# Kernel tuning notes

Measured on AMD Instinct MI355X. Metric: run time of the kernel, lower is better.

The kernel has to match this reference:

```python
import jax, jax.numpy as jnp
import numpy as np

DEN_LEAKY = 1e-05
NUM_LEAKY = 1e-20


def _chain_objf(xexp, lengths, e_in, e_out, e_pdf, e_prob, leaky, final, coeff):
    """Leaky-HMM forward recursion (pychain forward_backward objective).

    xexp: [B,T,D] exp'd clamped network outputs
    e_*:  edge lists, either shared [E] or per-utterance [B,E]
    leaky/final: [S] or [B,S]
    Returns scalar objf = sum_b log p(X_b | graph_b).
    """
    B, T, D = xexp.shape
    if leaky.ndim == 1:
        leaky = jnp.broadcast_to(leaky[None, :], (B, leaky.shape[0]))
        final = jnp.broadcast_to(final[None, :], (B, final.shape[0]))
    S = leaky.shape[1]
    if e_in.ndim == 1:
        E = e_in.shape[0]
        e_in = jnp.broadcast_to(e_in[None, :], (B, E))
        e_out = jnp.broadcast_to(e_out[None, :], (B, E))
        e_pdf = jnp.broadcast_to(e_pdf[None, :], (B, E))
        e_prob = jnp.broadcast_to(e_prob[None, :], (B, E))
    seg = (e_out + S * jnp.arange(B, dtype=e_out.dtype)[:, None]).ravel()

    # alpha at t=0: mass 1 on start_state (0), plus leaky mass (alpha_sum = 1)
    alpha0 = jnp.zeros((B, S), xexp.dtype).at[:, 0].set(1.0)
    alpha0 = alpha0 + coeff * leaky

    mask_t = jnp.arange(T)[:, None] < lengths[None, :]  # [T,B] ragged frame mask

    def step(carry, inp):
        alpha, logz = carry
        xt, m = inp  # xt: [B,D], m: [B]
        # transition scores: alpha[src] * graph_prob * exp_logit[pdf]
        vals = (jnp.take_along_axis(alpha, e_in, axis=1)
                * e_prob
                * jnp.take_along_axis(xt, e_pdf, axis=1))  # [B,E]
        anew = jax.ops.segment_sum(vals.ravel(), seg, num_segments=B * S).reshape(B, S)
        asum = anew.sum(-1, keepdims=True)  # [B,1] per-frame arbitrary scale
        adash = (anew + coeff * leaky * asum) / asum  # leaky-HMM + renorm
        alpha = jnp.where(m[:, None], adash, alpha)
        logz = logz + jnp.where(m, jnp.log(asum[:, 0]), 0.0)
        return (alpha, logz), None

    (alpha, logz), _ = jax.lax.scan(
        step, (alpha0, jnp.zeros((B,), xexp.dtype)),
        (jnp.transpose(xexp, (1, 0, 2)), mask_t))
    return jnp.sum(logz + jnp.log(jnp.sum(alpha * final, axis=-1)))


def setup_inputs() -> dict:
    key = jax.random.key(0)
    ks = jax.random.split(key, 12)
    B, T, D = 32, 400, 2048
    S_den, E_den = 2000, 60000
    S_num, E_num = 512, 2048
    x = jax.random.normal(ks[0], (B, T, D), dtype=jnp.float32)
    x_lengths = jnp.clip(T - jnp.arange(B, dtype=jnp.int32) * 8, 32, T)  # sorted desc
    den_e_in = jax.random.randint(ks[1], (E_den,), 0, S_den, dtype=jnp.int32)
    den_e_out = jax.random.randint(ks[2], (E_den,), 0, S_den, dtype=jnp.int32)
    den_e_pdf = jax.random.randint(ks[3], (E_den,), 0, D, dtype=jnp.int32)
    den_e_prob = jax.random.uniform(ks[4], (E_den,), dtype=jnp.float32, minval=0.05, maxval=1.0)
    den_leaky = jax.random.uniform(ks[5], (S_den,), dtype=jnp.float32, minval=0.01, maxval=1.0)
    den_final = jax.random.uniform(ks[6], (S_den,), dtype=jnp.float32, minval=0.1, maxval=1.0)
    num_e_in = jax.random.randint(ks[7], (B, E_num), 0, S_num, dtype=jnp.int32)
    num_e_out = jax.random.randint(ks[8], (B, E_num), 0, S_num, dtype=jnp.int32)
    num_e_pdf = jax.random.randint(ks[9], (B, E_num), 0, D, dtype=jnp.int32)
    num_e_prob = jax.random.uniform(ks[10], (B, E_num), dtype=jnp.float32, minval=0.05, maxval=1.0)
    k11, k12 = jax.random.split(ks[11])
    num_leaky = jax.random.uniform(k11, (B, S_num), dtype=jnp.float32, minval=0.01, maxval=1.0)
    num_final = jax.random.uniform(k12, (B, S_num), dtype=jnp.float32, minval=0.1, maxval=1.0)
    return {"x": x, "x_lengths": x_lengths,
            "den_e_in": den_e_in, "den_e_out": den_e_out, "den_e_pdf": den_e_pdf,
            "den_e_prob": den_e_prob, "den_leaky": den_leaky, "den_final": den_final,
            "num_e_in": num_e_in, "num_e_out": num_e_out, "num_e_pdf": num_e_pdf,
            "num_e_prob": num_e_prob, "num_leaky": num_leaky, "num_final": num_final}


def reference(x, x_lengths, den_e_in, den_e_out, den_e_pdf, den_e_prob, den_leaky,
              den_final, num_e_in, num_e_out, num_e_pdf, num_e_prob, num_leaky,
              num_final):
    xexp = jnp.exp(jnp.clip(x, -30.0, 30.0))
    den_objf = _chain_objf(xexp, x_lengths, den_e_in, den_e_out, den_e_pdf,
                           den_e_prob, den_leaky, den_final, DEN_LEAKY)
    num_objf = _chain_objf(xexp, x_lengths, num_e_in, num_e_out, num_e_pdf,
                           num_e_prob, num_leaky, num_final, NUM_LEAKY)
    objf = -(num_objf - den_objf)
    return objf / x_lengths.sum().astype(x.dtype)
```

## Files before the change

### kernel.cpp

```cpp
#include <hip/hip_runtime.h>
#include <math.h>

#define B_SZ   32
#define T_SZ   400
#define D_SZ   2048
#define S_DEN  2000
#define E_DEN  60000
#define S_NUM  512
#define E_NUM  2048
#define DEN_C  1e-5f
#define NUM_C  1e-20f

#define P_CH   4
#define NTHR   512
#define EPT    32
#define EPC    16384

#define REC_OFF     0u
#define ANEWG_OFF   0u
#define PACK_OFF    960000u
#define ROWPTR_OFF  1484288u
#define CNT_OFF     1492352u
#define SROW_OFF    1492352u
#define CUR_OFF     1500352u
#define RSPLIT_OFF  1508352u
#define PSUM_OFF    1508416u
#define CTR_OFF     1509440u
#define TOTD_OFF    1509568u
#define TOTN_OFF    1509696u
#define WS_BYTES    1509824u

__device__ __forceinline__ float expclip(float v) {
    return __expf(fminf(fmaxf(v, -30.f), 30.f));
}
__device__ __forceinline__ float ldf_agent(const float* p) {
    return __hip_atomic_load(p, __ATOMIC_RELAXED, __HIP_MEMORY_SCOPE_AGENT);
}
__device__ __forceinline__ int ldi_agent(const int* p) {
    return __hip_atomic_load(p, __ATOMIC_RELAXED, __HIP_MEMORY_SCOPE_AGENT);
}
__device__ __forceinline__ void stf_agent(float* p, float v) {
    __hip_atomic_store(p, v, __ATOMIC_RELAXED, __HIP_MEMORY_SCOPE_AGENT);
}

__global__ void prep_init(char* ws) {
    int tid = threadIdx.x;
    int* cnt = (int*)(ws + CNT_OFF);
    int* cur = (int*)(ws + CUR_OFF);
    for (int i = tid; i < S_DEN; i += 256) { cnt[i] = 0; cur[i] = 0; }
    if (tid < B_SZ) ((int*)(ws + CTR_OFF))[tid] = 0;
}

__global__ void prep_hist(const int* __restrict__ e_out, char* ws) {
    int e = blockIdx.x * blockDim.x + threadIdx.x;
    if (e < E_DEN) atomicAdd((int*)(ws + CNT_OFF) + e_out[e], 1);
}

__global__ __launch_bounds__(1024) void prep_scan(char* ws) {
    __shared__ int sb[2][2048];
    const int* cnt = (const int*)(ws + CNT_OFF);
    int* rowp = (int*)(ws + ROWPTR_OFF);
    int tid = threadIdx.x;
    for (int i = tid; i < 2048; i += 1024) sb[0][i] = (i < S_DEN) ? cnt[i] : 0;
    __syncthreads();
    int cur = 0;
    for (int d = 1; d < 2048; d <<= 1) {
        for (int i = tid; i < 2048; i += 1024)
            sb[1 - cur][i] = sb[cur][i] + ((i >= d) ? sb[cur][i - d] : 0);
        __syncthreads();
        cur ^= 1;
    }
    if (tid == 0) rowp[0] = 0;
    for (int i = tid; i < S_DEN; i += 1024) rowp[i + 1] = sb[cur][i];
    __syncthreads();
    if (tid == 0) {
        int* rs = (int*)(ws + RSPLIT_OFF);
        rs[0] = 0; rs[P_CH] = S_DEN;
        for (int p = 1; p < P_CH; ++p) {
            int target = (E_DEN / P_CH) * p;
            int lo = 0, hi = S_DEN;
            while (lo < hi) {
                int mid = (lo + hi) >> 1;
                int v = (mid == 0) ? 0 : sb[cur][mid - 1];
                if (v >= target) hi = mid; else lo = mid + 1;
            }
            rs[p] = lo;
        }
    }
}

__global__ void prep_scatter(const int* __restrict__ e_in, const int* __restrict__ e_out,
                             const int* __restrict__ e_pdf, const float* __restrict__ e_prob,
                             char* ws) {
    int e = blockIdx.x * blockDim.x + threadIdx.x;
    if (e >= E_DEN) return;
    const int* rowp = (const int*)(ws + ROWPTR_OFF);
    int* cur = (int*)(ws + CUR_OFF);
    int4* recs = (int4*)(ws + REC_OFF);
    int o = e_out[e];
    int pos = rowp[o] + atomicAdd(&cur[o], 1);
    int4 r;
    r.x = e_in[e]; r.y = e_pdf[e];
    r.z = __float_as_int(e_prob[e]);
    r.w = o;
    recs[pos] = r;
}

__global__ void prep_pack(char* ws) {
    int slot = blockIdx.x * blockDim.x + threadIdx.x;
    if (slot >= P_CH * EPC) return;
    int p = slot >> 14;
    int k = slot & (EPC - 1);
    const int* rowp = (const int*)(ws + ROWPTR_OFF);
    const int* rs = (const int*)(ws + RSPLIT_OFF);
    int ebase = rowp[rs[p]], eend = rowp[rs[p + 1]];
    uint2* pk = (uint2*)(ws + PACK_OFF);
    int idx = ebase + k;
    uint2 val;
    int myrow;
    if (idx < eend) {
        const int4* r4 = (const int4*)(ws + REC_OFF);
        int4 r = r4[idx];
        myrow = r.w;
        int nxt = (idx + 1 < eend) ? r4[idx + 1].w : myrow;
        unsigned d = (unsigned)(nxt - myrow);
        if (d > 1023u) d = 1023u;
        val = make_uint2((unsigned)r.x | ((unsigned)r.y << 11) | (d << 22),
                         (unsigned)r.z);
    } else {
        val = make_uint2(0u, 0u);
        myrow = rs[p];
    }
    pk[slot] = val;
    if ((k & (EPT - 1)) == 0)
        ((int*)(ws + SROW_OFF))[(p << 9) + (k >> 5)] = myrow;
}

__global__ __launch_bounds__(NTHR, 2) void chain_fwd3(
    const float* __restrict__ x, const int* __restrict__ lengths,
    const float* __restrict__ den_leaky, const float* __restrict__ den_final,
    const int* __restrict__ num_in, const int* __restrict__ num_out,
    const int* __restrict__ num_pdf, const float* __restrict__ num_prob,
    const float* __restrict__ num_leaky, const float* __restrict__ num_final,
    char* __restrict__ ws)
{
    __shared__ float alpha[2048];
    __shared__ float xrow[2048];
    __shared__ float anew[2048];
    __shared__ float red[8];
    extern __shared__ float dynpad[];
    const int tid = threadIdx.x;
    if (lengths[0] == -12345) dynpad[tid] = 1.f;

    if (blockIdx.x < P_CH * B_SZ) {
        const int b = blockIdx.x & (B_SZ - 1);
        const int p = blockIdx.x >> 5;
        const int len = lengths[b];
        const float* xb = x + (size_t)b * T_SZ * D_SZ;
        const int* rs = (const int*)(ws + RSPLIT_OFF);
        const int rlo = rs[p], rhi = rs[p + 1];
        float* anewg = (float*)(ws + ANEWG_OFF) + ((size_t)(b << 1) << 11);
        float* psumg = (float*)(ws + PSUM_OFF);
        int* ctr = (int*)(ws + CTR_OFF) + b;

        float lc[4], fc[4];
        #pragma unroll
        for (int i = 0; i < 4; ++i) {
            int s = tid + (i << 9);
            lc[i] = (s < S_DEN) ? DEN_C * den_leaky[s] : 0.f;
            fc[i] = (s < S_DEN) ? den_final[s] : 0.f;
        }
        #pragma unroll
        for (int i = 0; i < 4; ++i) {
            int s = tid + (i << 9);
            alpha[s] = lc[i] + ((s == 0) ? 1.f : 0.f);
            anew[s] = 0.f;
            xrow[s] = expclip(xb[s]);
        }

        const uint4* __restrict__ pk4 = (const uint4*)(ws + PACK_OFF);
        const int qb = (p << 13) + (tid << 4);
        const int row0 = ((const int*)(ws + SROW_OFF))[(p << 9) + tid];
        float logz = 0.f;
        uint4 c0 = pk4[qb + 0], c1 = pk4[qb + 1], c2 = pk4[qb + 2], c3 = pk4[qb + 3];
        uint4 c4 = pk4[qb + 4], c5 = pk4[qb + 5], c6 = pk4[qb + 6], c7 = pk4[qb + 7];
        __syncthreads();

        for (int t = 0; t < len; ++t) {
            const int tn = (t + 1 < len) ? t + 1 : t;
            const float* xq = xb + (size_t)tn * D_SZ;
            const float xn0 = xq[tid], xn1 = xq[tid + 512];
            const float xn2 = xq[tid + 1024], xn3 = xq[tid + 1536];

            float acc = 0.f, psum = 0.f;
            int row = row0;
            #pragma unroll
            for (int sb = 0; sb < 2; ++sb) {
                const int nq = qb + (((sb + 1) & 1) << 3);
                uint4 n0 = pk4[nq + 0], n1 = pk4[nq + 1], n2 = pk4[nq + 2], n3 = pk4[nq + 3];
                uint4 n4 = pk4[nq + 4], n5 = pk4[nq + 5], n6 = pk4[nq + 6], n7 = pk4[nq + 7];
                const unsigned w[16] = {c0.x, c0.z, c1.x, c1.z, c2.x, c2.z, c3.x, c3.z,
                                        c4.x, c4.z, c5.x, c5.z, c6.x, c6.z, c7.x, c7.z};
                const unsigned pr[16] = {c0.y, c0.w, c1.y, c1.w, c2.y, c2.w, c3.y, c3.w,
                                         c4.y, c4.w, c5.y, c5.w, c6.y, c6.w, c7.y, c7.w};
                float av[16], xv[16];
                #pragma unroll
                for (int i = 0; i < 16; ++i) av[i] = alpha[w[i] & 2047u];
                #pragma unroll
                for (int i = 0; i < 16; ++i) xv[i] = xrow[(w[i] >> 11) & 2047u];
                #pragma unroll
                for (int i = 0; i < 16; ++i) {
                    acc = __fmaf_rn(av[i] * __uint_as_float(pr[i]), xv[i], acc);
                    const unsigned d = w[i] >> 22;
                    if (d) { psum += acc; atomicAdd(&anew[row], acc); acc = 0.f; row += (int)d; }
                }
                c0 = n0; c1 = n1; c2 = n2; c3 = n3;
                c4 = n4; c5 = n5; c6 = n6; c7 = n7;
            }
            psum += acc;
            if (acc != 0.f) atomicAdd(&anew[row], acc);

            #pragma unroll
            for (int o = 32; o > 0; o >>= 1) psum += __shfl_down(psum, o, 64);
            if ((tid & 63) == 0) red[tid >> 6] = psum;
            __syncthreads();

            float* ag = anewg + ((t & 1) << 11);
            const int pbase = ((b << 1) | (t & 1)) * P_CH;
            if (tid == 0) {
                float bs = 0.f;
                #pragma unroll
                for (int i = 0; i < 8; ++i) bs += red[i];
                stf_agent(&psumg[pbase + p], bs);
            }
            for (int r = rlo + tid; r < rhi; r += NTHR) { stf_agent(&ag[r], anew[r]); anew[r] = 0.f; }
            asm volatile("s_waitcnt vmcnt(0)" ::: "memory");
            __syncthreads();
            if (tid == 0) {
                __hip_atomic_fetch_add(ctr, 1, __ATOMIC_RELAXED, __HIP_MEMORY_SCOPE_AGENT);
                const int target = P_CH * (t + 1);
                int guard = 0;
                while (ldi_agent(ctr) < target) {
                    __builtin_amdgcn_s_sleep(2);
                    if (++guard > (1 << 17)) break;
                }
            }
            __syncthreads();

            float asum = 0.f;
            #pragma unroll
            for (int q = 0; q < P_CH; ++q) asum += ldf_agent(&psumg[pbase + q]);
            const float inv = 1.f / asum;

            #pragma unroll
            for (int i = 0; i < 4; ++i) {
                const int s = tid + (i << 9);
                float an = (s < S_DEN) ? ldf_agent(&ag[s]) : 0.f;
                alpha[s] = __fmaf_rn(an, inv, lc[i]);
            }
            xrow[tid]        = expclip(xn0);
            xrow[tid + 512]  = expclip(xn1);
            xrow[tid + 1024] = expclip(xn2);
            xrow[tid + 1536] = expclip(xn3);
            logz += logf(asum);
            __syncthreads();
        }

        if (p == 0) {
            float fs = alpha[tid] * fc[0] + alpha[tid + 512] * fc[1]
                     + alpha[tid + 1024] * fc[2] + alpha[tid + 1536] * fc[3];
            #pragma unroll
            for (int o = 32; o > 0; o >>= 1) fs += __shfl_down(fs, o, 64);
            if ((tid & 63) == 0) red[tid >> 6] = fs;
            __syncthreads();
            if (tid == 0) {
                float tot = 0.f;
                #pragma unroll
                for (int i = 0; i < 8; ++i) tot += red[i];
                ((float*)(ws + TOTD_OFF))[b] = logz + logf(tot);
            }
        }
    } else {
        const int b = blockIdx.x - P_CH * B_SZ;
        const int len = lengths[b];
        const float* xb = x + (size_t)b * T_SZ * D_SZ;
        float* nalpha = alpha;
        float* nanew  = anew;
        const float lk = num_leaky[(b << 9) + tid];
        const float fn = num_final[(b << 9) + tid];
        int ein[4], eout[4], epdf[4]; float eprb[4];
        #pragma unroll
        for (int k = 0; k < 4; ++k) {
            int e = (b << 11) + tid + (k << 9);
            ein[k] = num_in[e]; eout[k] = num_out[e];
            epdf[k] = num_pdf[e]; eprb[k] = num_prob[e];
        }
        nalpha[tid] = NUM_C * lk + ((tid == 0) ? 1.f : 0.f);
        nanew[tid] = 0.f;
        #pragma unroll
        for (int i = 0; i < 4; ++i) xrow[tid + (i << 9)] = expclip(xb[tid + (i << 9)]);
        float logz = 0.f;
        __syncthreads();

        for (int t = 0; t < len; ++t) {
            const int tn = (t + 1 < len) ? t + 1 : t;
            const float* xq = xb + (size_t)tn * D_SZ;
            const float xn0 = xq[tid], xn1 = xq[tid + 512];
            const float xn2 = xq[tid + 1024], xn3 = xq[tid + 1536];
            #pragma unroll
            for (int k = 0; k < 4; ++k) {
                float v = nalpha[ein[k]] * eprb[k] * xrow[epdf[k]];
                atomicAdd(&nanew[eout[k]], v);
            }
            __syncthreads();
            float ps = nanew[tid];
            #pragma unroll
            for (int o = 32; o > 0; o >>= 1) ps += __shfl_down(ps, o, 64);
            if ((tid & 63) == 0) red[tid >> 6] = ps;
            __syncthreads();
            float asum = 0.f;
            #pragma unroll
            for (int i = 0; i < 8; ++i) asum += red[i];
            nalpha[tid] = __fmaf_rn(NUM_C * lk, asum, nanew[tid]) * (1.f / asum);
            nanew[tid] = 0.f;
            xrow[tid]        = expclip(xn0);
            xrow[tid + 512]  = expclip(xn1);
            xrow[tid + 1024] = expclip(xn2);
            xrow[tid + 1536] = expclip(xn3);
            logz += logf(asum);
            __syncthreads();
        }
        float fs = nalpha[tid] * fn;
        #pragma unroll
        for (int o = 32; o > 0; o >>= 1) fs += __shfl_down(fs, o, 64);
        if ((tid & 63) == 0) red[tid >> 6] = fs;
        __syncthreads();
        if (tid == 0) {
            float tot = 0.f;
            #pragma unroll
            for (int i = 0; i < 8; ++i) tot += red[i];
            ((float*)(ws + TOTN_OFF))[b] = logz + logf(tot);
        }
    }
}

__global__ void combine2(const char* __restrict__ ws, const int* __restrict__ lengths,
                         float* __restrict__ out) {
    const float* totd = (const float*)(ws + TOTD_OFF);
    const float* totn = (const float*)(ws + TOTN_OFF);
    int tid = threadIdx.x;
    float v = 0.f, l = 0.f;
    if (tid < B_SZ) { v = totd[tid] - totn[tid]; l = (float)lengths[tid]; }
    #pragma unroll
    for (int o = 32; o > 0; o >>= 1) { v += __shfl_down(v, o, 64); l += __shfl_down(l, o, 64); }
    if (tid == 0) out[0] = v / l;
}

__global__ __launch_bounds__(1024) void chain_fwd_kernel(
    const float* __restrict__ x, const int* __restrict__ lengths,
    const int* __restrict__ den_in, const int* __restrict__ den_out,
    const int* __restrict__ den_pdf, const float* __restrict__ den_prob,
    const float* __restrict__ den_leaky, const float* __restrict__ den_final,
    const int* __restrict__ num_in, const int* __restrict__ num_out,
    const int* __restrict__ num_pdf, const float* __restrict__ num_prob,
    const float* __restrict__ num_leaky, const float* __restrict__ num_final,
    float* __restrict__ part)
{
    __shared__ float xrow[D_SZ];
    __shared__ float alpha[S_DEN];
    __shared__ float anew[S_DEN];
    __shared__ float red[17];
    const int tid = threadIdx.x;
    const int nthr = 1024;
    const bool is_den = blockIdx.x < B_SZ;
    const int b = blockIdx.x & (B_SZ - 1);
    int S, E;
    const int *e_in, *e_out, *e_pdf;
    const float *e_prob, *leaky, *fin;
    float coeff;
    if (is_den) {
        S = S_DEN; E = E_DEN;
        e_in = den_in; e_out = den_out; e_pdf = den_pdf; e_prob = den_prob;
        leaky = den_leaky; fin = den_final; coeff = DEN_C;
    } else {
        S = S_NUM; E = E_NUM;
        e_in = num_in + b * E_NUM; e_out = num_out + b * E_NUM;
        e_pdf = num_pdf + b * E_NUM; e_prob = num_prob + b * E_NUM;
        leaky = num_leaky + b * S_NUM; fin = num_final + b * S_NUM;
        coeff = NUM_C;
    }
    const int len = lengths[b];
    const float* xb = x + (size_t)b * T_SZ * D_SZ;
    for (int s = tid; s < S; s += nthr)
        alpha[s] = coeff * leaky[s] + (s == 0 ? 1.0f : 0.0f);
    float logz = 0.0f;
    for (int t = 0; t < len; ++t) {
        for (int s = tid; s < S; s += nthr) anew[s] = 0.0f;
        const float* xt = xb + (size_t)t * D_SZ;
        for (int d = tid; d < D_SZ; d += nthr)
            xrow[d] = __expf(fminf(fmaxf(xt[d], -30.0f), 30.0f));
        __syncthreads();
        for (int e = tid; e < E; e += nthr) {
            float v = alpha[e_in[e]] * e_prob[e] * xrow[e_pdf[e]];
            atomicAdd(&anew[e_out[e]], v);
        }
        __syncthreads();
        float ps = 0.0f;
        for (int s = tid; s < S; s += nthr) ps += anew[s];
        #pragma unroll
        for (int off = 32; off > 0; off >>= 1) ps += __shfl_down(ps, off, 64);
        if ((tid & 63) == 0) red[tid >> 6] = ps;
        __syncthreads();
        if (tid < 64) {
            float v = (tid < 16) ? red[tid] : 0.0f;
            #pragma unroll
            for (int off = 8; off > 0; off >>= 1) v += __shfl_down(v, off, 64);
            if (tid == 0) red[16] = v;
        }
        __syncthreads();
        const float asum = red[16];
        const float inv = 1.0f / asum;
        for (int s = tid; s < S; s += nthr)
            alpha[s] = (anew[s] + coeff * leaky[s] * asum) * inv;
        logz += logf(asum);
        __syncthreads();
    }
    float fs = 0.0f;
    for (int s = tid; s < S; s += nthr) fs += alpha[s] * fin[s];
    #pragma unroll
    for (int off = 32; off > 0; off >>= 1) fs += __shfl_down(fs, off, 64);
    if ((tid & 63) == 0) red[tid >> 6] = fs;
    __syncthreads();
    if (tid < 64) {
        float v = (tid < 16) ? red[tid] : 0.0f;
        #pragma unroll
        for (int off = 8; off > 0; off >>= 1) v += __shfl_down(v, off, 64);
        if (tid == 0) part[blockIdx.x] = logz + logf(v);
    }
}

__global__ void combine_kernel(const float* __restrict__ part,
                               const int* __restrict__ lengths,
                               float* __restrict__ out)
{
    int tid = threadIdx.x;
    float v = 0.0f, l = 0.0f;
    if (tid < B_SZ) { v = part[tid] - part[B_SZ + tid]; l = (float)lengths[tid]; }
    #pragma unroll
    for (int off = 32; off > 0; off >>= 1) { v += __shfl_down(v, off, 64); l += __shfl_down(l, off, 64); }
    if (tid == 0) out[0] = v / l;
}

extern "C" void kernel_launch(void* const* d_in, const int* in_sizes, int n_in,
                              void* d_out, int out_size, void* d_ws, size_t ws_size,
                              hipStream_t stream)
{
    const float* x          = (const float*)d_in[0];
    const int*   lengths    = (const int*)  d_in[1];
    const int*   den_in_p   = (const int*)  d_in[2];
    const int*   den_out_p  = (const int*)  d_in[3];
    const int*   den_pdf_p  = (const int*)  d_in[4];
    const float* den_prob_p = (const float*)d_in[5];
    const float* den_leaky  = (const float*)d_in[6];
    const float* den_final  = (const float*)d_in[7];
    const int*   num_in_p   = (const int*)  d_in[8];
    const int*   num_out_p  = (const int*)  d_in[9];
    const int*   num_pdf_p  = (const int*)  d_in[10];
    const float* num_prob_p = (const float*)d_in[11];
    const float* num_leaky  = (const float*)d_in[12];
    const float* num_final  = (const float*)d_in[13];

    if (ws_size >= WS_BYTES) {
        char* ws = (char*)d_ws;
        hipLaunchKernelGGL(prep_init, dim3(1), dim3(256), 0, stream, ws);
        hipLaunchKernelGGL(prep_hist, dim3((E_DEN + 255) / 256), dim3(256), 0, stream,
                           den_out_p, ws);
        hipLaunchKernelGGL(prep_scan, dim3(1), dim3(1024), 0, stream, ws);
        hipLaunchKernelGGL(prep_scatter, dim3((E_DEN + 255) / 256), dim3(256), 0, stream,
                           den_in_p, den_out_p, den_pdf_p, den_prob_p, ws);
        hipLaunchKernelGGL(prep_pack, dim3((P_CH * EPC + 255) / 256), dim3(256), 0, stream, ws);
        hipLaunchKernelGGL(chain_fwd3, dim3(P_CH * B_SZ + B_SZ), dim3(NTHR), 60000, stream,
                           x, lengths, den_leaky, den_final,
                           num_in_p, num_out_p, num_pdf_p, num_prob_p,
                           num_leaky, num_final, ws);
        hipLaunchKernelGGL(combine2, dim3(1), dim3(64), 0, stream,
                           ws, lengths, (float*)d_out);
    } else {
        float* part = (float*)d_ws;
        hipLaunchKernelGGL(chain_fwd_kernel, dim3(2 * B_SZ), dim3(1024), 0, stream,
                           x, lengths,
                           den_in_p, den_out_p, den_pdf_p, den_prob_p, den_leaky, den_final,
                           num_in_p, num_out_p, num_pdf_p, num_prob_p, num_leaky, num_final,
                           part);
        hipLaunchKernelGGL(combine_kernel, dim3(1), dim3(64), 0, stream,
                           part, lengths, (float*)d_out);
    }
}
```

Baseline: 2.785 ms.

## Interleave two utterances per denominator block with per-block ready flags

Each denominator block now runs the recursion for a pair of utterances in lockstep. It does both edge passes before waiting on the cross-block partial sums, so the wait for one utterance is hidden behind work on the other. The shared arrival counter is replaced by per-partition monotonic step flags, and the partial sums are polled by a few lanes. This halves the number of denominator blocks and doubles shared-memory state per block. The loop runs for the first utterance's length, so it assumes the second utterance in each pair is no longer than the first.

```diff
diff --git a/kernel.cpp b/kernel.cpp
--- a/kernel.cpp
+++ b/kernel.cpp
@@ -12,6 +12,7 @@
 #define NUM_C  1e-20f
 
 #define P_CH   4
+#define PGRP   16
 #define NTHR   512
 #define EPT    32
 #define EPC    16384
@@ -25,10 +26,10 @@
 #define CUR_OFF     1500352u
 #define RSPLIT_OFF  1508352u
 #define PSUM_OFF    1508416u
-#define CTR_OFF     1509440u
-#define TOTD_OFF    1509568u
-#define TOTN_OFF    1509696u
-#define WS_BYTES    1509824u
+#define FLAG_OFF    1509440u
+#define TOTD_OFF    1509952u
+#define TOTN_OFF    1510080u
+#define WS_BYTES    1510208u
 
 __device__ __forceinline__ float expclip(float v) {
     return __expf(fminf(fmaxf(v, -30.f), 30.f));
@@ -40,6 +41,9 @@
     return __hip_atomic_load(p, __ATOMIC_RELAXED, __HIP_MEMORY_SCOPE_AGENT);
 }
 __device__ __forceinline__ void stf_agent(float* p, float v) {
+    __hip_atomic_store(p, v, __ATOMIC_RELAXED, __HIP_MEMORY_SCOPE_AGENT);
+}
+__device__ __forceinline__ void sti_agent(int* p, int v) {
     __hip_atomic_store(p, v, __ATOMIC_RELAXED, __HIP_MEMORY_SCOPE_AGENT);
 }
 
@@ -48,7 +52,8 @@
     int* cnt = (int*)(ws + CNT_OFF);
     int* cur = (int*)(ws + CUR_OFF);
     for (int i = tid; i < S_DEN; i += 256) { cnt[i] = 0; cur[i] = 0; }
-    if (tid < B_SZ) ((int*)(ws + CTR_OFF))[tid] = 0;
+    int* flags = (int*)(ws + FLAG_OFF);
+    if (tid < B_SZ * P_CH) flags[tid] = 0;
 }
 
 __global__ void prep_hist(const int* __restrict__ e_out, char* ws) {
@@ -136,7 +141,41 @@
         ((int*)(ws + SROW_OFF))[(p << 9) + (k >> 5)] = myrow;
 }
 
-__global__ __launch_bounds__(NTHR, 2) void chain_fwd3(
+#define EDGE_PASS(ALD, XLD, NLD)                                               \
+  {                                                                            \
+    float acc = 0.f, psum = 0.f;                                               \
+    int row = row0;                                                            \
+    _Pragma("unroll")                                                          \
+    for (int sb = 0; sb < 2; ++sb) {                                           \
+      const int nq = qb + (((sb + 1) & 1) << 3);                               \
+      uint4 n0 = pk4[nq + 0], n1 = pk4[nq + 1], n2 = pk4[nq + 2], n3 = pk4[nq + 3]; \
+      uint4 n4 = pk4[nq + 4], n5 = pk4[nq + 5], n6 = pk4[nq + 6], n7 = pk4[nq + 7]; \
+      const unsigned w[16] = {c0.x, c0.z, c1.x, c1.z, c2.x, c2.z, c3.x, c3.z,  \
+                              c4.x, c4.z, c5.x, c5.z, c6.x, c6.z, c7.x, c7.z}; \
+      const unsigned pr[16] = {c0.y, c0.w, c1.y, c1.w, c2.y, c2.w, c3.y, c3.w, \
+                               c4.y, c4.w, c5.y, c5.w, c6.y, c6.w, c7.y, c7.w};\
+      float av[16], xv[16];                                                    \
+      _Pragma("unroll")                                                        \
+      for (int i = 0; i < 16; ++i) av[i] = (ALD)[w[i] & 2047u];                \
+      _Pragma("unroll")                                                        \
+      for (int i = 0; i < 16; ++i) xv[i] = (XLD)[(w[i] >> 11) & 2047u];        \
+      _Pragma("unroll")                                                        \
+      for (int i = 0; i < 16; ++i) {                                           \
+        acc = __fmaf_rn(av[i] * __uint_as_float(pr[i]), xv[i], acc);           \
+        const unsigned d = w[i] >> 22;                                         \
+        if (d) { psum += acc; atomicAdd(&(NLD)[row], acc); acc = 0.f; row += (int)d; } \
+      }                                                                        \
+      c0 = n0; c1 = n1; c2 = n2; c3 = n3;                                      \
+      c4 = n4; c5 = n5; c6 = n6; c7 = n7;                                      \
+    }                                                                          \
+    psum += acc;                                                               \
+    if (acc != 0.f) atomicAdd(&(NLD)[row], acc);                               \
+    _Pragma("unroll")                                                          \
+    for (int o = 32; o > 0; o >>= 1) psum += __shfl_down(psum, o, 64);         \
+    if ((tid & 63) == 0) red[tid >> 6] = psum;                                 \
+  }
+
+__global__ __launch_bounds__(NTHR, 2) void chain_fwd4(
     const float* __restrict__ x, const int* __restrict__ lengths,
     const float* __restrict__ den_leaky, const float* __restrict__ den_final,
     const int* __restrict__ num_in, const int* __restrict__ num_out,
@@ -144,24 +183,26 @@
     const float* __restrict__ num_leaky, const float* __restrict__ num_final,
     char* __restrict__ ws)
 {
-    __shared__ float alpha[2048];
-    __shared__ float xrow[2048];
-    __shared__ float anew[2048];
-    __shared__ float red[8];
+    __shared__ float sAlpha[2][2048];
+    __shared__ float sXrow[2][2048];
+    __shared__ float sAnew[2][2048];
+    __shared__ float red[16];
     extern __shared__ float dynpad[];
     const int tid = threadIdx.x;
     if (lengths[0] == -12345) dynpad[tid] = 1.f;
 
-    if (blockIdx.x < P_CH * B_SZ) {
-        const int b = blockIdx.x & (B_SZ - 1);
-        const int p = blockIdx.x >> 5;
-        const int len = lengths[b];
-        const float* xb = x + (size_t)b * T_SZ * D_SZ;
+    if (blockIdx.x < P_CH * PGRP) {
+        const int g = blockIdx.x & (PGRP - 1);
+        const int p = blockIdx.x >> 4;
+        const int bA = 2 * g, bB = 2 * g + 1;
+        const int lenA = lengths[bA], lenB = lengths[bB];
+        const float* xA = x + (size_t)bA * T_SZ * D_SZ;
+        const float* xB = x + (size_t)bB * T_SZ * D_SZ;
         const int* rs = (const int*)(ws + RSPLIT_OFF);
         const int rlo = rs[p], rhi = rs[p + 1];
-        float* anewg = (float*)(ws + ANEWG_OFF) + ((size_t)(b << 1) << 11);
+        float* anewg = (float*)(ws + ANEWG_OFF);
         float* psumg = (float*)(ws + PSUM_OFF);
-        int* ctr = (int*)(ws + CTR_OFF) + b;
+        int* flags   = (int*)(ws + FLAG_OFF);
 
         float lc[4], fc[4];
         #pragma unroll
@@ -173,119 +214,152 @@
         #pragma unroll
         for (int i = 0; i < 4; ++i) {
             int s = tid + (i << 9);
-            alpha[s] = lc[i] + ((s == 0) ? 1.f : 0.f);
-            anew[s] = 0.f;
-            xrow[s] = expclip(xb[s]);
+            float a0 = lc[i] + ((s == 0) ? 1.f : 0.f);
+            sAlpha[0][s] = a0; sAlpha[1][s] = a0;
+            sAnew[0][s] = 0.f; sAnew[1][s] = 0.f;
+            sXrow[0][s] = expclip(xA[s]);
+            sXrow[1][s] = expclip(xB[s]);
         }
 
         const uint4* __restrict__ pk4 = (const uint4*)(ws + PACK_OFF);
         const int qb = (p << 13) + (tid << 4);
         const int row0 = ((const int*)(ws + SROW_OFF))[(p << 9) + tid];
-        float logz = 0.f;
+        float logzA = 0.f, logzB = 0.f;
         uint4 c0 = pk4[qb + 0], c1 = pk4[qb + 1], c2 = pk4[qb + 2], c3 = pk4[qb + 3];
         uint4 c4 = pk4[qb + 4], c5 = pk4[qb + 5], c6 = pk4[qb + 6], c7 = pk4[qb + 7];
         __syncthreads();
 
-        for (int t = 0; t < len; ++t) {
-            const int tn = (t + 1 < len) ? t + 1 : t;
-            const float* xq = xb + (size_t)tn * D_SZ;
-            const float xn0 = xq[tid], xn1 = xq[tid + 512];
-            const float xn2 = xq[tid + 1024], xn3 = xq[tid + 1536];
-
-            float acc = 0.f, psum = 0.f;
-            int row = row0;
+        for (int t = 0; t < lenA; ++t) {
+            const bool haveB = (t < lenB);
+            const int par = t & 1;
+
+            const int tnA = (t + 1 < lenA) ? t + 1 : t;
+            const float* xqA = xA + (size_t)tnA * D_SZ;
+            const float xa0 = xqA[tid],        xa1 = xqA[tid + 512];
+            const float xa2 = xqA[tid + 1024], xa3 = xqA[tid + 1536];
+            float xb0 = 0.f, xb1 = 0.f, xb2 = 0.f, xb3 = 0.f;
+            if (haveB) {
+                const int tnB = (t + 1 < lenB) ? t + 1 : t;
+                const float* xqB = xB + (size_t)tnB * D_SZ;
+                xb0 = xqB[tid];        xb1 = xqB[tid + 512];
+                xb2 = xqB[tid + 1024]; xb3 = xqB[tid + 1536];
+            }
+
+            EDGE_PASS(sAlpha[0], sXrow[0], sAnew[0]);
+            __syncthreads();
+            {
+                float* ag = anewg + (size_t)(((bA << 1) | par) << 11);
+                if (tid == 0) {
+                    float bs = red[0]+red[1]+red[2]+red[3]+red[4]+red[5]+red[6]+red[7];
+                    stf_agent(&psumg[(((bA << 1) | par) << 2) + p], bs);
+                }
+                for (int r = rlo + tid; r < rhi; r += NTHR) {
+                    stf_agent(&ag[r], sAnew[0][r]); sAnew[0][r] = 0.f;
+                }
+                asm volatile("s_waitcnt vmcnt(0)" ::: "memory");
+            }
+            __syncthreads();
+            if (tid == 0) sti_agent(&flags[(bA << 2) + p], t + 1);
+
+            if (haveB) {
+                EDGE_PASS(sAlpha[1], sXrow[1], sAnew[1]);
+                __syncthreads();
+                {
+                    float* ag = anewg + (size_t)(((bB << 1) | par) << 11);
+                    if (tid == 0) {
+                        float bs = red[0]+red[1]+red[2]+red[3]+red[4]+red[5]+red[6]+red[7];
+                        stf_agent(&psumg[(((bB << 1) | par) << 2) + p], bs);
+                    }
+                    for (int r = rlo + tid; r < rhi; r += NTHR) {
+                        stf_agent(&ag[r], sAnew[1][r]); sAnew[1][r] = 0.f;
+                    }
+                    asm volatile("s_waitcnt vmcnt(0)" ::: "memory");
+                }
+                __syncthreads();
+                if (tid == 0) sti_agent(&flags[(bB << 2) + p], t + 1);
+            }
+
+            sXrow[0][tid]        = expclip(xa0);
+            sXrow[0][tid + 512]  = expclip(xa1);
+            sXrow[0][tid + 1024] = expclip(xa2);
+            sXrow[0][tid + 1536] = expclip(xa3);
+            if (haveB) {
+                sXrow[1][tid]        = expclip(xb0);
+                sXrow[1][tid + 512]  = expclip(xb1);
+                sXrow[1][tid + 1024] = expclip(xb2);
+                sXrow[1][tid + 1536] = expclip(xb3);
+            }
+
+            if (tid < 4) {
+                const int fi = (bA << 2) + tid; int gd = 0;
+                while (ldi_agent(&flags[fi]) < t + 1) {
+                    __builtin_amdgcn_s_sleep(1);
+                    if (++gd > (1 << 15)) break;
+                }
+                red[8 + tid] = ldf_agent(&psumg[(((bA << 1) | par) << 2) + tid]);
+            } else if (haveB && tid >= 64 && tid < 68) {
+                const int q = tid - 64;
+                const int fi = (bB << 2) + q; int gd = 0;
+                while (ldi_agent(&flags[fi]) < t + 1) {
+                    __builtin_amdgcn_s_sleep(1);
+                    if (++gd > (1 << 15)) break;
+                }
+                red[12 + q] = ldf_agent(&psumg[(((bB << 1) | par) << 2) + q]);
+            }
+            __syncthreads();
+
+            {
+                const float asum = red[8] + red[9] + red[10] + red[11];
+                const float inv = 1.f / asum;
+                const float* ag = anewg + (size_t)(((bA << 1) | par) << 11);
+                #pragma unroll
+                for (int i = 0; i < 4; ++i) {
+                    const int s = tid + (i << 9);
+                    float an = (s < S_DEN) ? ldf_agent(&ag[s]) : 0.f;
+                    sAlpha[0][s] = __fmaf_rn(an, inv, lc[i]);
+                }
+                logzA += logf(asum);
+            }
+            if (haveB) {
+                const float asum = red[12] + red[13] + red[14] + red[15];
+                const float inv = 1.f / asum;
+                const float* ag = anewg + (size_t)(((bB << 1) | par) << 11);
+                #pragma unroll
+                for (int i = 0; i < 4; ++i) {
+                    const int s = tid + (i << 9);
+                    float an = (s < S_DEN) ? ldf_agent(&ag[s]) : 0.f;
+                    sAlpha[1][s] = __fmaf_rn(an, inv, lc[i]);
+                }
+                logzB += logf(asum);
+            }
+            __syncthreads();
+        }
+
+        if (p == 0) {
             #pragma unroll
-            for (int sb = 0; sb < 2; ++sb) {
-                const int nq = qb + (((sb + 1) & 1) << 3);
-                uint4 n0 = pk4[nq + 0], n1 = pk4[nq + 1], n2 = pk4[nq + 2], n3 = pk4[nq + 3];
-                uint4 n4 = pk4[nq + 4], n5 = pk4[nq + 5], n6 = pk4[nq + 6], n7 = pk4[nq + 7];
-                const unsigned w[16] = {c0.x, c0.z, c1.x, c1.z, c2.x, c2.z, c3.x, c3.z,
-                                        c4.x, c4.z, c5.x, c5.z, c6.x, c6.z, c7.x, c7.z};
-                const unsigned pr[16] = {c0.y, c0.w, c1.y, c1.w, c2.y, c2.w, c3.y, c3.w,
-                                         c4.y, c4.w, c5.y, c5.w, c6.y, c6.w, c7.y, c7.w};
-                float av[16], xv[16];
+            for (int u = 0; u < 2; ++u) {
+                const int b = (u == 0) ? bA : bB;
+                const float logz = (u == 0) ? logzA : logzB;
+                float fs = sAlpha[u][tid] * fc[0] + sAlpha[u][tid + 512] * fc[1]
+                         + sAlpha[u][tid + 1024] * fc[2] + sAlpha[u][tid + 1536] * fc[3];
                 #pragma unroll
-                for (int i = 0; i < 16; ++i) av[i] = alpha[w[i] & 2047u];
-                #pragma unroll
-                for (int i = 0; i < 16; ++i) xv[i] = xrow[(w[i] >> 11) & 2047u];
-                #pragma unroll
-                for (int i = 0; i < 16; ++i) {
-                    acc = __fmaf_rn(av[i] * __uint_as_float(pr[i]), xv[i], acc);
-                    const unsigned d = w[i] >> 22;
-                    if (d) { psum += acc; atomicAdd(&anew[row], acc); acc = 0.f; row += (int)d; }
-                }
-                c0 = n0; c1 = n1; c2 = n2; c3 = n3;
-                c4 = n4; c5 = n5; c6 = n6; c7 = n7;
-            }
-            psum += acc;
-            if (acc != 0.f) atomicAdd(&anew[row], acc);
-
-            #pragma unroll
-            for (int o = 32; o > 0; o >>= 1) psum += __shfl_down(psum, o, 64);
-            if ((tid & 63) == 0) red[tid >> 6] = psum;
-            __syncthreads();
-
-            float* ag = anewg + ((t & 1) << 11);
-            const int pbase = ((b << 1) | (t & 1)) * P_CH;
-            if (tid == 0) {
-                float bs = 0.f;
-                #pragma unroll
-                for (int i = 0; i < 8; ++i) bs += red[i];
-                stf_agent(&psumg[pbase + p], bs);
-            }
-            for (int r = rlo + tid; r < rhi; r += NTHR) { stf_agent(&ag[r], anew[r]); anew[r] = 0.f; }
-            asm volatile("s_waitcnt vmcnt(0)" ::: "memory");
-            __syncthreads();
-            if (tid == 0) {
-                __hip_atomic_fetch_add(ctr, 1, __ATOMIC_RELAXED, __HIP_MEMORY_SCOPE_AGENT);
-                const int target = P_CH * (t + 1);
-                int guard = 0;
-                while (ldi_agent(ctr) < target) {
-                    __builtin_amdgcn_s_sleep(2);
-                    if (++guard > (1 << 17)) break;
-                }
-            }
-            __syncthreads();
-
-            float asum = 0.f;
-            #pragma unroll
-            for (int q = 0; q < P_CH; ++q) asum += ldf_agent(&psumg[pbase + q]);
-            const float inv = 1.f / asum;
-
-            #pragma unroll
-            for (int i = 0; i < 4; ++i) {
-                const int s = tid + (i << 9);
-                float an = (s < S_DEN) ? ldf_agent(&ag[s]) : 0.f;
-                alpha[s] = __fmaf_rn(an, inv, lc[i]);
-            }
-            xrow[tid]        = expclip(xn0);
-            xrow[tid + 512]  = expclip(xn1);
-            xrow[tid + 1024] = expclip(xn2);
-            xrow[tid + 1536] = expclip(xn3);
-            logz += logf(asum);
-            __syncthreads();
-        }
-
-        if (p == 0) {
-            float fs = alpha[tid] * fc[0] + alpha[tid + 512] * fc[1]
-                     + alpha[tid + 1024] * fc[2] + alpha[tid + 1536] * fc[3];
-            #pragma unroll
-            for (int o = 32; o > 0; o >>= 1) fs += __shfl_down(fs, o, 64);
-            if ((tid & 63) == 0) red[tid >> 6] = fs;
-            __syncthreads();
-            if (tid == 0) {
-                float tot = 0.f;
-                #pragma unroll
-                for (int i = 0; i < 8; ++i) tot += red[i];
-                ((float*)(ws + TOTD_OFF))[b] = logz + logf(tot);
+                for (int o = 32; o > 0; o >>= 1) fs += __shfl_down(fs, o, 64);
+                if ((tid & 63) == 0) red[tid >> 6] = fs;
+                __syncthreads();
+                if (tid == 0) {
+                    float tot = red[0]+red[1]+red[2]+red[3]+red[4]+red[5]+red[6]+red[7];
+                    ((float*)(ws + TOTD_OFF))[b] = logz + logf(tot);
+                }
+                __syncthreads();
             }
         }
     } else {
-        const int b = blockIdx.x - P_CH * B_SZ;
+        const int b = blockIdx.x - P_CH * PGRP;
         const int len = lengths[b];
         const float* xb = x + (size_t)b * T_SZ * D_SZ;
-        float* nalpha = alpha;
-        float* nanew  = anew;
+        float* nalpha = &sAlpha[0][0];
+        float* nanew  = &sAnew[0][0];
+        float* xrow   = &sXrow[0][0];
         const float lk = num_leaky[(b << 9) + tid];
         const float fn = num_final[(b << 9) + tid];
         int ein[4], eout[4], epdf[4]; float eprb[4];
@@ -479,7 +553,7 @@
         hipLaunchKernelGGL(prep_scatter, dim3((E_DEN + 255) / 256), dim3(256), 0, stream,
                            den_in_p, den_out_p, den_pdf_p, den_prob_p, ws);
         hipLaunchKernelGGL(prep_pack, dim3((P_CH * EPC + 255) / 256), dim3(256), 0, stream, ws);
-        hipLaunchKernelGGL(chain_fwd3, dim3(P_CH * B_SZ + B_SZ), dim3(NTHR), 60000, stream,
+        hipLaunchKernelGGL(chain_fwd4, dim3(P_CH * PGRP + B_SZ), dim3(NTHR), 40960, stream,
                            x, lengths, den_leaky, den_final,
                            num_in_p, num_out_p, num_pdf_p, num_prob_p,
                            num_leaky, num_final, ws);
```

After: 4.775 ms. 71.4% more time.

## Restructure cross-block barrier: per-wave arrivals, padded counters, overlap xrow update

Applied to the files above, without the earlier changes.

Each wave now signals the per-utterance counter after its own stores, which removes one block-wide __syncthreads before the arrival. Only the first wave spins on the counter, and it also reads the partial sums into shared memory. The exp of the next x row is moved ahead of the spin wait so it overlaps the wait. Counters are padded to separate 64-byte slots and partial-sum slots are spread out to cut false sharing. In exchange there are more atomics per step and a shorter spin guard.

```diff
diff --git a/kernel.cpp b/kernel.cpp
--- a/kernel.cpp
+++ b/kernel.cpp
@@ -25,10 +25,10 @@
 #define CUR_OFF     1500352u
 #define RSPLIT_OFF  1508352u
 #define PSUM_OFF    1508416u
-#define CTR_OFF     1509440u
-#define TOTD_OFF    1509568u
-#define TOTN_OFF    1509696u
-#define WS_BYTES    1509824u
+#define CTR_OFF     1510464u
+#define TOTD_OFF    1512512u
+#define TOTN_OFF    1512640u
+#define WS_BYTES    1512768u
 
 __device__ __forceinline__ float expclip(float v) {
     return __expf(fminf(fmaxf(v, -30.f), 30.f));
@@ -48,7 +48,7 @@
     int* cnt = (int*)(ws + CNT_OFF);
     int* cur = (int*)(ws + CUR_OFF);
     for (int i = tid; i < S_DEN; i += 256) { cnt[i] = 0; cur[i] = 0; }
-    if (tid < B_SZ) ((int*)(ws + CTR_OFF))[tid] = 0;
+    if (tid < B_SZ) ((int*)(ws + CTR_OFF))[tid << 4] = 0;
 }
 
 __global__ void prep_hist(const int* __restrict__ e_out, char* ws) {
@@ -136,7 +136,7 @@
         ((int*)(ws + SROW_OFF))[(p << 9) + (k >> 5)] = myrow;
 }
 
-__global__ __launch_bounds__(NTHR, 2) void chain_fwd3(
+__global__ __launch_bounds__(NTHR, 2) void chain_fwd5(
     const float* __restrict__ x, const int* __restrict__ lengths,
     const float* __restrict__ den_leaky, const float* __restrict__ den_final,
     const int* __restrict__ num_in, const int* __restrict__ num_out,
@@ -147,7 +147,7 @@
     __shared__ float alpha[2048];
     __shared__ float xrow[2048];
     __shared__ float anew[2048];
-    __shared__ float red[8];
+    __shared__ float red[16];
     extern __shared__ float dynpad[];
     const int tid = threadIdx.x;
     if (lengths[0] == -12345) dynpad[tid] = 1.f;
@@ -161,7 +161,7 @@
         const int rlo = rs[p], rhi = rs[p + 1];
         float* anewg = (float*)(ws + ANEWG_OFF) + ((size_t)(b << 1) << 11);
         float* psumg = (float*)(ws + PSUM_OFF);
-        int* ctr = (int*)(ws + CTR_OFF) + b;
+        int* ctr = (int*)(ws + CTR_OFF) + (b << 4);
 
         float lc[4], fc[4];
         #pragma unroll
@@ -187,6 +187,7 @@
         __syncthreads();
 
         for (int t = 0; t < len; ++t) {
+            const int par = t & 1;
             const int tn = (t + 1 < len) ? t + 1 : t;
             const float* xq = xb + (size_t)tn * D_SZ;
             const float xn0 = xq[tid], xn1 = xq[tid + 512];
@@ -225,43 +226,43 @@
             if ((tid & 63) == 0) red[tid >> 6] = psum;
             __syncthreads();
 
-            float* ag = anewg + ((t & 1) << 11);
-            const int pbase = ((b << 1) | (t & 1)) * P_CH;
+            float* ag = anewg + (par << 11);
+            const int pidx = (b << 4) | (par << 3);
             if (tid == 0) {
-                float bs = 0.f;
-                #pragma unroll
-                for (int i = 0; i < 8; ++i) bs += red[i];
-                stf_agent(&psumg[pbase + p], bs);
-            }
-            for (int r = rlo + tid; r < rhi; r += NTHR) { stf_agent(&ag[r], anew[r]); anew[r] = 0.f; }
+                float bs = red[0]+red[1]+red[2]+red[3]+red[4]+red[5]+red[6]+red[7];
+                stf_agent(&psumg[pidx + p], bs);
+            }
+            for (int r = rlo + tid; r < rhi; r += NTHR) {
+                stf_agent(&ag[r], anew[r]); anew[r] = 0.f;
+            }
             asm volatile("s_waitcnt vmcnt(0)" ::: "memory");
-            __syncthreads();
-            if (tid == 0) {
+            if ((tid & 63) == 0)
                 __hip_atomic_fetch_add(ctr, 1, __ATOMIC_RELAXED, __HIP_MEMORY_SCOPE_AGENT);
-                const int target = P_CH * (t + 1);
-                int guard = 0;
+
+            xrow[tid]        = expclip(xn0);
+            xrow[tid + 512]  = expclip(xn1);
+            xrow[tid + 1024] = expclip(xn2);
+            xrow[tid + 1536] = expclip(xn3);
+
+            if (tid < 64) {
+                const int target = (P_CH * (NTHR / 64)) * (t + 1);
+                int gd = 0;
                 while (ldi_agent(ctr) < target) {
-                    __builtin_amdgcn_s_sleep(2);
-                    if (++guard > (1 << 17)) break;
+                    __builtin_amdgcn_s_sleep(1);
+                    if (++gd > (1 << 15)) break;
                 }
-            }
-            __syncthreads();
-
-            float asum = 0.f;
-            #pragma unroll
-            for (int q = 0; q < P_CH; ++q) asum += ldf_agent(&psumg[pbase + q]);
+                if (tid < 4) red[8 + tid] = ldf_agent(&psumg[pidx + tid]);
+            }
+            __syncthreads();
+
+            const float asum = red[8] + red[9] + red[10] + red[11];
             const float inv = 1.f / asum;
-
             #pragma unroll
             for (int i = 0; i < 4; ++i) {
                 const int s = tid + (i << 9);
                 float an = (s < S_DEN) ? ldf_agent(&ag[s]) : 0.f;
                 alpha[s] = __fmaf_rn(an, inv, lc[i]);
             }
-            xrow[tid]        = expclip(xn0);
-            xrow[tid + 512]  = expclip(xn1);
-            xrow[tid + 1024] = expclip(xn2);
-            xrow[tid + 1536] = expclip(xn3);
             logz += logf(asum);
             __syncthreads();
         }
@@ -274,9 +275,7 @@
             if ((tid & 63) == 0) red[tid >> 6] = fs;
             __syncthreads();
             if (tid == 0) {
-                float tot = 0.f;
-                #pragma unroll
-                for (int i = 0; i < 8; ++i) tot += red[i];
+                float tot = red[0]+red[1]+red[2]+red[3]+red[4]+red[5]+red[6]+red[7];
                 ((float*)(ws + TOTD_OFF))[b] = logz + logf(tot);
             }
         }
@@ -479,7 +478,7 @@
         hipLaunchKernelGGL(prep_scatter, dim3((E_DEN + 255) / 256), dim3(256), 0, stream,
                            den_in_p, den_out_p, den_pdf_p, den_prob_p, ws);
         hipLaunchKernelGGL(prep_pack, dim3((P_CH * EPC + 255) / 256), dim3(256), 0, stream, ws);
-        hipLaunchKernelGGL(chain_fwd3, dim3(P_CH * B_SZ + B_SZ), dim3(NTHR), 60000, stream,
+        hipLaunchKernelGGL(chain_fwd5, dim3(P_CH * B_SZ + B_SZ), dim3(NTHR), 60000, stream,
                            x, lengths, den_leaky, den_final,
                            num_in_p, num_out_p, num_pdf_p, num_prob_p,
                            num_leaky, num_final, ws);
```

Result: no change. 2.792 ms (+0.2%).
